# Kernel tuning notes

Measured on AMD Instinct MI355X. Metric: run time of the kernel, lower is better.

## Reference

```python
import jax, jax.numpy as jnp
import numpy as np

B, S, D, E = 4, 4096, 2048, 64
NOISE_STD = 1.0


def setup_inputs() -> dict:
    key = jax.random.key(0)
    k1, k2, k3, k4 = jax.random.split(key, 4)
    x = jax.random.normal(k1, (B, S, D), dtype=jnp.float32)
    lim = float(np.sqrt(6.0 / (D + E)))  # glorot_uniform
    W_gate = jax.random.uniform(k2, (D, E), jnp.float32, -lim, lim)
    # keras inits noise_dense kernel to zeros; use tiny random values so the
    # noise path is numerically exercised (zeros would make it trivially ln(2)).
    W_noise = 0.02 * jax.random.normal(k3, (D, E), dtype=jnp.float32)
    noise = jax.random.normal(k4, (B * S, E), dtype=jnp.float32)
    return {"x": x, "W_gate": W_gate, "W_noise": W_noise, "noise": noise, "top_k": 2}


def reference(x, W_gate, W_noise, noise, top_k):
    b, s, d = x.shape
    e = W_gate.shape[1]
    xf = x.reshape(-1, d)                         # [N, D], N = b*s
    gate_logits = xf @ W_gate                     # [N, E]
    # training-mode noise injection
    noise_logits = xf @ W_noise                   # [N, E]
    nstd = jax.nn.softplus(noise_logits) * (NOISE_STD / (e * e))
    gate_logits = gate_logits + noise * nstd
    # top-k mask + masked softmax
    top_vals, top_idx = jax.lax.top_k(gate_logits, top_k)   # [N, K]
    n = gate_logits.shape[0]
    mask = jnp.zeros_like(gate_logits).at[jnp.arange(n)[:, None], top_idx].set(1.0)
    masked_logits = jnp.where(mask > 0, gate_logits, jnp.float32(-1e9))
    expert_weights = jax.nn.softmax(masked_logits, axis=-1)  # [N, E]
    raw_gate_probs = jax.nn.softmax(gate_logits, axis=-1)    # [N, E]
    expert_weights = expert_weights.reshape(b, s, e)
    expert_indices = top_idx.reshape(b, s, top_k).astype(jnp.int32)
    return expert_weights, expert_indices, gate_logits, raw_gate_probs
```

## Files before the change

kernel.cpp:

```cpp
#include <hip/hip_runtime.h>
#include <math.h>


typedef _Float16 f16;
typedef f16  f16x8  __attribute__((ext_vector_type(8)));
typedef float f32x16 __attribute__((ext_vector_type(16)));

constexpr int NROWS = 16384;
constexpr int DDIM  = 2048;
constexpr int NE    = 64;
constexpr int BM    = 32;
constexpr int KI    = 32;
constexpr int NITER = DDIM / KI;
constexpr float NSCALE = 1.0f / 4096.0f;

__device__ __forceinline__ float softplus_f(float x) {
    return fmaxf(x, 0.0f) + log1pf(expf(-fabsf(x)));
}

__device__ __forceinline__ int a_off(int buf, int v, int s) {
    return ((buf * 2 + v) * 2 + s) * 1024;
}
__device__ __forceinline__ int b_off(int buf, int v, int f, int s) {
    return 8192 + (((buf * 2 + v) * 4 + f) * 2 + s) * 1024;
}

__device__ __forceinline__ void gload_lds16(const void* g, void* l) {
    __builtin_amdgcn_global_load_lds(
        (const __attribute__((address_space(1))) void*)g,
        (__attribute__((address_space(3))) void*)l, 16, 0, 0);
}

__global__ __launch_bounds__(256) void wprep_kernel(
    const float* __restrict__ Wg, const float* __restrict__ Wn,
    f16* __restrict__ ws)
{
    int t = blockIdx.x * 256 + threadIdx.x;
    int S = t >> 8;
    int f = (t >> 6) & 3;
    int l = t & 63;
    int k0  = S * 16 + (l >> 5) * 8;
    int col = f * 32 + (l & 31);
    const float* src = (col < NE) ? (Wg + col) : (Wn + col - NE);
    f16x8 hp, lp;
    #pragma unroll
    for (int j = 0; j < 8; ++j) {
        float w  = src[(size_t)(k0 + j) * NE];
        f16 h    = (f16)w;
        float hf = (float)h;
        hp[j] = h;
        lp[j] = (f16)((w - hf) * 64.0f);
    }
    size_t base = (size_t)(S * 4 + f) * 1024;
    *(f16x8*)(ws + base + l * 8)       = hp;
    *(f16x8*)(ws + base + 512 + l * 8) = lp;
}

__global__ __launch_bounds__(256, 2) void gemm_gating(
    const float* __restrict__ x, const f16* __restrict__ wfrag,
    const float* __restrict__ noise,
    float* __restrict__ out_w, float* __restrict__ out_idx,
    float* __restrict__ out_logits, float* __restrict__ out_probs)
{
    __shared__ char smem[40960];
    const int tid = threadIdx.x;
    const int l   = tid & 63;
    const int w   = tid >> 6;
    const int row0 = blockIdx.x * BM;

    f32x16 acc1, acc2;
    #pragma unroll
    for (int r = 0; r < 16; ++r) { acc1[r] = 0.0f; acc2[r] = 0.0f; }

    const int sA   = w;
    const int sr   = l & 31;
    const int kg   = sA * 2 + (l >> 5);
    const float* xrow = x + (size_t)(row0 + sr) * DDIM + kg * 8;

    float4 xv0, xv1;
    auto stageA_load = [&](int i) {
        if (w < 2) {
            xv0 = *(const float4*)(xrow + i * KI);
            xv1 = *(const float4*)(xrow + i * KI + 4);
        }
    };
    auto stageA_write = [&](int buf) {
        if (w < 2) {
            float xs[8] = {xv0.x, xv0.y, xv0.z, xv0.w, xv1.x, xv1.y, xv1.z, xv1.w};
            f16x8 hp, lp;
            #pragma unroll
            for (int j = 0; j < 8; ++j) {
                f16 h    = (f16)xs[j];
                float hf = (float)h;
                hp[j] = h;
                lp[j] = (f16)((xs[j] - hf) * 64.0f);
            }
            *(f16x8*)(smem + a_off(buf, 0, sA) + l * 16) = hp;
            *(f16x8*)(smem + a_off(buf, 1, sA) + l * 16) = lp;
        }
    };
    auto stageB = [&](int i, int buf) {
        #pragma unroll
        for (int v = 0; v < 2; ++v)
            #pragma unroll
            for (int s = 0; s < 2; ++s) {
                int S = i * 2 + s;
                const f16* src = wfrag + (size_t)(S * 4 + w) * 1024 + v * 512 + l * 8;
                gload_lds16(src, smem + b_off(buf, v, w, s));
            }
    };
    auto compute = [&](int buf) {
        #pragma unroll
        for (int s = 0; s < 2; ++s) {
            f16x8 Ah = *(const f16x8*)(smem + a_off(buf, 0, s) + l * 16);
            f16x8 Al = *(const f16x8*)(smem + a_off(buf, 1, s) + l * 16);
            f16x8 Bh = *(const f16x8*)(smem + b_off(buf, 0, w, s) + l * 16);
            f16x8 Bl = *(const f16x8*)(smem + b_off(buf, 1, w, s) + l * 16);
            acc1 = __builtin_amdgcn_mfma_f32_32x32x16_f16(Ah, Bh, acc1, 0, 0, 0);
            acc2 = __builtin_amdgcn_mfma_f32_32x32x16_f16(Ah, Bl, acc2, 0, 0, 0);
            acc2 = __builtin_amdgcn_mfma_f32_32x32x16_f16(Al, Bh, acc2, 0, 0, 0);
        }
    };

    stageA_load(0);
    stageB(0, 0);
    stageA_write(0);
    __syncthreads();

    for (int i = 0; i < NITER; ++i) {
        int buf = i & 1;
        bool more = (i + 1 < NITER);
        if (more) { stageA_load(i + 1); stageB(i + 1, buf ^ 1); }
        compute(buf);
        if (more) stageA_write(buf ^ 1);
        __syncthreads();
    }

    float* lgf = (float*)smem;
    #pragma unroll
    for (int r = 0; r < 16; ++r) {
        float cv = fmaf(acc2[r], 0.015625f, acc1[r]);
        int row = (r & 3) + 8 * (r >> 2) + 4 * (l >> 5);
        int col = w * 32 + (l & 31);
        lgf[row * 132 + col] = cv;
    }
    __syncthreads();

    {
        const int pr = tid & 31;
        const int c8 = tid >> 5;
        const int n1 = row0 + pr;
        const float4* gl4 = (const float4*)(lgf + pr * 132 + c8 * 8);
        const float4* nl4 = (const float4*)(lgf + pr * 132 + 64 + c8 * 8);
        const float4* nz4 = (const float4*)(noise + (size_t)n1 * NE + c8 * 8);
        float4* gw4 = (float4*)(lgf + pr * 132 + c8 * 8);
        float4* ol4 = (float4*)(out_logits + (size_t)n1 * NE + c8 * 8);
        #pragma unroll
        for (int q = 0; q < 2; ++q) {
            float4 G = gl4[q], NL = nl4[q], NZ = nz4[q];
            G.x += NZ.x * softplus_f(NL.x) * NSCALE;
            G.y += NZ.y * softplus_f(NL.y) * NSCALE;
            G.z += NZ.z * softplus_f(NL.z) * NSCALE;
            G.w += NZ.w * softplus_f(NL.w) * NSCALE;
            gw4[q] = G;
            ol4[q] = G;
        }
    }
    __syncthreads();

    {
        const int g2   = l >> 3;
        const int c    = l & 7;
        const int row2 = w * 8 + g2;
        const int n2   = row0 + row2;

        float mv[8];
        {
            const float4* mr = (const float4*)(lgf + row2 * 132 + c * 8);
            float4 m0 = mr[0], m1 = mr[1];
            mv[0]=m0.x; mv[1]=m0.y; mv[2]=m0.z; mv[3]=m0.w;
            mv[4]=m1.x; mv[5]=m1.y; mv[6]=m1.z; mv[7]=m1.w;
        }
        float v0 = -INFINITY, v1 = -INFINITY;
        int i0 = 0, i1 = 0;
        #pragma unroll
        for (int j = 0; j < 8; ++j) {
            float v = mv[j]; int e = c * 8 + j;
            if (v > v0) { v1 = v0; i1 = i0; v0 = v; i0 = e; }
            else if (v > v1) { v1 = v; i1 = e; }
        }
        #pragma unroll
        for (int m = 1; m <= 4; m <<= 1) {
            float ov0 = __shfl_xor(v0, m), ov1 = __shfl_xor(v1, m);
            int   oi0 = __shfl_xor(i0, m), oi1 = __shfl_xor(i1, m);
            if (ov0 > v0) {
                bool keep = (v0 > ov1);
                v1 = keep ? v0 : ov1; i1 = keep ? i0 : oi1;
                v0 = ov0; i0 = oi0;
            } else if (ov0 > v1) {
                v1 = ov0; i1 = oi0;
            }
        }
        const int srcl = l & 56;
        v0 = __shfl(v0, srcl); i0 = __shfl(i0, srcl);
        v1 = __shfl(v1, srcl); i1 = __shfl(i1, srcl);

        float se = 0.0f;
        #pragma unroll
        for (int j = 0; j < 8; ++j) se += expf(mv[j] - v0);
        se += __shfl_xor(se, 1); se += __shfl_xor(se, 2); se += __shfl_xor(se, 4);
        float inv_se = 1.0f / se;

        float t  = expf(v1 - v0);
        float w0 = 1.0f / (1.0f + t);
        float w1 = t * w0;

        float pr[8], wt[8];
        #pragma unroll
        for (int j = 0; j < 8; ++j) {
            int e = c * 8 + j;
            pr[j] = expf(mv[j] - v0) * inv_se;
            wt[j] = (e == i0) ? w0 : ((e == i1) ? w1 : 0.0f);
        }
        *(float4*)(out_probs + (size_t)n2 * NE + c * 8)     = make_float4(pr[0], pr[1], pr[2], pr[3]);
        *(float4*)(out_probs + (size_t)n2 * NE + c * 8 + 4) = make_float4(pr[4], pr[5], pr[6], pr[7]);
        *(float4*)(out_w + (size_t)n2 * NE + c * 8)         = make_float4(wt[0], wt[1], wt[2], wt[3]);
        *(float4*)(out_w + (size_t)n2 * NE + c * 8 + 4)     = make_float4(wt[4], wt[5], wt[6], wt[7]);
        if (c == 0) {
            *(float2*)(out_idx + (size_t)n2 * 2) = make_float2((float)i0, (float)i1);
        }
    }
}

extern "C" void kernel_launch(void* const* d_in, const int* in_sizes, int n_in,
                              void* d_out, int out_size, void* d_ws, size_t ws_size,
                              hipStream_t stream) {
    (void)in_sizes; (void)n_in; (void)ws_size; (void)out_size;
    const float* x     = (const float*)d_in[0];
    const float* Wg    = (const float*)d_in[1];
    const float* Wn    = (const float*)d_in[2];
    const float* noise = (const float*)d_in[3];
    float* out        = (float*)d_out;
    float* out_w      = out;
    float* out_idx    = out + (size_t)NROWS * NE;
    float* out_logits = out_idx + (size_t)NROWS * 2;
    float* out_probs  = out_logits + (size_t)NROWS * NE;
    f16* wfrag = (f16*)d_ws;

    wprep_kernel<<<128, 256, 0, stream>>>(Wg, Wn, wfrag);
    gemm_gating<<<NROWS / BM, 256, 0, stream>>>(
        x, wfrag, noise, out_w, out_idx, out_logits, out_probs);
}
```

Baseline: 63.20 us.

## Replace LDS-staged double buffering with direct register loads for GEMM operands

The GEMM main loop no longer stages x and weight fragments through shared memory with per-iteration barriers. Each wave now loads its A and B fragments straight from global memory into registers, using a two-deep software prefetch, and does the fp16 hi/lo split in registers. This removes the LDS traffic and the __syncthreads in the loop. The cost is that all four waves now load the same x rows redundantly, and global-load latency is hidden only by register prefetch.

```diff
diff --git a/kernel.cpp b/kernel.cpp
--- a/kernel.cpp
+++ b/kernel.cpp
@@ -10,25 +10,11 @@
 constexpr int DDIM  = 2048;
 constexpr int NE    = 64;
 constexpr int BM    = 32;
-constexpr int KI    = 32;
-constexpr int NITER = DDIM / KI;
+constexpr int NSL   = DDIM / 16;
 constexpr float NSCALE = 1.0f / 4096.0f;
 
 __device__ __forceinline__ float softplus_f(float x) {
     return fmaxf(x, 0.0f) + log1pf(expf(-fabsf(x)));
-}
-
-__device__ __forceinline__ int a_off(int buf, int v, int s) {
-    return ((buf * 2 + v) * 2 + s) * 1024;
-}
-__device__ __forceinline__ int b_off(int buf, int v, int f, int s) {
-    return 8192 + (((buf * 2 + v) * 4 + f) * 2 + s) * 1024;
-}
-
-__device__ __forceinline__ void gload_lds16(const void* g, void* l) {
-    __builtin_amdgcn_global_load_lds(
-        (const __attribute__((address_space(1))) void*)g,
-        (__attribute__((address_space(3))) void*)l, 16, 0, 0);
 }
 
 __global__ __launch_bounds__(256) void wprep_kernel(
@@ -62,7 +48,7 @@
     float* __restrict__ out_w, float* __restrict__ out_idx,
     float* __restrict__ out_logits, float* __restrict__ out_probs)
 {
-    __shared__ char smem[40960];
+    __shared__ float lgf[BM * 132];
     const int tid = threadIdx.x;
     const int l   = tid & 63;
     const int w   = tid >> 6;
@@ -72,71 +58,52 @@
     #pragma unroll
     for (int r = 0; r < 16; ++r) { acc1[r] = 0.0f; acc2[r] = 0.0f; }
 
-    const int sA   = w;
-    const int sr   = l & 31;
-    const int kg   = sA * 2 + (l >> 5);
-    const float* xrow = x + (size_t)(row0 + sr) * DDIM + kg * 8;
-
-    float4 xv0, xv1;
-    auto stageA_load = [&](int i) {
-        if (w < 2) {
-            xv0 = *(const float4*)(xrow + i * KI);
-            xv1 = *(const float4*)(xrow + i * KI + 4);
-        }
+    const float* aptr = x + (size_t)(row0 + (l & 31)) * DDIM + ((l >> 5) * 8);
+    const f16*   bptr = wfrag + (size_t)w * 1024 + l * 8;
+
+    auto loadA = [&](int S, float4& a0, float4& a1) {
+        const float* p = aptr + S * 16;
+        a0 = *(const float4*)p;
+        a1 = *(const float4*)(p + 4);
     };
-    auto stageA_write = [&](int buf) {
-        if (w < 2) {
-            float xs[8] = {xv0.x, xv0.y, xv0.z, xv0.w, xv1.x, xv1.y, xv1.z, xv1.w};
-            f16x8 hp, lp;
-            #pragma unroll
-            for (int j = 0; j < 8; ++j) {
-                f16 h    = (f16)xs[j];
-                float hf = (float)h;
-                hp[j] = h;
-                lp[j] = (f16)((xs[j] - hf) * 64.0f);
-            }
-            *(f16x8*)(smem + a_off(buf, 0, sA) + l * 16) = hp;
-            *(f16x8*)(smem + a_off(buf, 1, sA) + l * 16) = lp;
-        }
+    auto loadB = [&](int S, f16x8& bh, f16x8& bl) {
+        const f16* p = bptr + (size_t)S * 4096;
+        bh = *(const f16x8*)p;
+        bl = *(const f16x8*)(p + 512);
     };
-    auto stageB = [&](int i, int buf) {
-        #pragma unroll
-        for (int v = 0; v < 2; ++v)
-            #pragma unroll
-            for (int s = 0; s < 2; ++s) {
-                int S = i * 2 + s;
-                const f16* src = wfrag + (size_t)(S * 4 + w) * 1024 + v * 512 + l * 8;
-                gload_lds16(src, smem + b_off(buf, v, w, s));
-            }
+    auto compute = [&](const float4& a0, const float4& a1,
+                       const f16x8& bh, const f16x8& bl) {
+        float xs[8] = {a0.x, a0.y, a0.z, a0.w, a1.x, a1.y, a1.z, a1.w};
+        f16x8 Ah, Al;
+        #pragma unroll
+        for (int j = 0; j < 8; ++j) {
+            f16 h    = (f16)xs[j];
+            float hf = (float)h;
+            Ah[j] = h;
+            Al[j] = (f16)((xs[j] - hf) * 64.0f);
+        }
+        acc1 = __builtin_amdgcn_mfma_f32_32x32x16_f16(Ah, bh, acc1, 0, 0, 0);
+        acc2 = __builtin_amdgcn_mfma_f32_32x32x16_f16(Ah, bl, acc2, 0, 0, 0);
+        acc2 = __builtin_amdgcn_mfma_f32_32x32x16_f16(Al, bh, acc2, 0, 0, 0);
     };
-    auto compute = [&](int buf) {
-        #pragma unroll
-        for (int s = 0; s < 2; ++s) {
-            f16x8 Ah = *(const f16x8*)(smem + a_off(buf, 0, s) + l * 16);
-            f16x8 Al = *(const f16x8*)(smem + a_off(buf, 1, s) + l * 16);
-            f16x8 Bh = *(const f16x8*)(smem + b_off(buf, 0, w, s) + l * 16);
-            f16x8 Bl = *(const f16x8*)(smem + b_off(buf, 1, w, s) + l * 16);
-            acc1 = __builtin_amdgcn_mfma_f32_32x32x16_f16(Ah, Bh, acc1, 0, 0, 0);
-            acc2 = __builtin_amdgcn_mfma_f32_32x32x16_f16(Ah, Bl, acc2, 0, 0, 0);
-            acc2 = __builtin_amdgcn_mfma_f32_32x32x16_f16(Al, Bh, acc2, 0, 0, 0);
-        }
-    };
-
-    stageA_load(0);
-    stageB(0, 0);
-    stageA_write(0);
-    __syncthreads();
-
-    for (int i = 0; i < NITER; ++i) {
-        int buf = i & 1;
-        bool more = (i + 1 < NITER);
-        if (more) { stageA_load(i + 1); stageB(i + 1, buf ^ 1); }
-        compute(buf);
-        if (more) stageA_write(buf ^ 1);
-        __syncthreads();
-    }
-
-    float* lgf = (float*)smem;
+
+    float4 ra0, ra1, sa0, sa1;
+    f16x8  rbh, rbl, sbh, sbl;
+    loadA(0, ra0, ra1);
+    loadB(0, rbh, rbl);
+
+    #pragma unroll 2
+    for (int t = 0; t < NSL / 2; ++t) {
+        loadA(2 * t + 1, sa0, sa1);
+        loadB(2 * t + 1, sbh, sbl);
+        compute(ra0, ra1, rbh, rbl);
+        if (t + 1 < NSL / 2) {
+            loadA(2 * t + 2, ra0, ra1);
+            loadB(2 * t + 2, rbh, rbl);
+        }
+        compute(sa0, sa1, sbh, sbl);
+    }
+
     #pragma unroll
     for (int r = 0; r < 16; ++r) {
         float cv = fmaf(acc2[r], 0.015625f, acc1[r]);
```

Result: slower. 88.84 us (+40.6%).

## Triple-buffer LDS pipeline with explicit vmcnt waits and split barriers

Applied to the files above, without the earlier changes.

Switches the main GEMM loop from double to triple buffering in LDS, prefetching the A and B tiles two iterations ahead. Hand-placed s_waitcnt vmcnt counts and sched barriers let async global-to-LDS loads stay in flight across barriers instead of draining every iteration. This raises LDS use from 40 KB to 60 KB per block, which may limit the two-blocks-per-CU occupancy target. It also relies on exact in-flight load counts being correct for each wave type.

```diff
diff --git a/kernel.cpp b/kernel.cpp
--- a/kernel.cpp
+++ b/kernel.cpp
@@ -19,16 +19,38 @@
 }
 
 __device__ __forceinline__ int a_off(int buf, int v, int s) {
-    return ((buf * 2 + v) * 2 + s) * 1024;
+    return buf * 4096 + (v * 2 + s) * 1024;
 }
 __device__ __forceinline__ int b_off(int buf, int v, int f, int s) {
-    return 8192 + (((buf * 2 + v) * 4 + f) * 2 + s) * 1024;
+    return 12288 + buf * 16384 + (((v * 4) + f) * 2 + s) * 1024;
 }
 
 __device__ __forceinline__ void gload_lds16(const void* g, void* l) {
     __builtin_amdgcn_global_load_lds(
         (const __attribute__((address_space(1))) void*)g,
         (__attribute__((address_space(3))) void*)l, 16, 0, 0);
+}
+
+__device__ __forceinline__ void barrier_close() {
+    asm volatile("s_waitcnt lgkmcnt(0)" ::: "memory");
+    __builtin_amdgcn_sched_barrier(0);
+    __builtin_amdgcn_s_barrier();
+    asm volatile("" ::: "memory");
+}
+__device__ __forceinline__ void barrier_publish_steady(bool heavy) {
+    if (heavy) asm volatile("s_waitcnt vmcnt(6) lgkmcnt(0)" ::: "memory");
+    else       asm volatile("s_waitcnt vmcnt(4) lgkmcnt(0)" ::: "memory");
+    __builtin_amdgcn_sched_barrier(0);
+    __builtin_amdgcn_s_barrier();
+    asm volatile("" ::: "memory");
+    __builtin_amdgcn_sched_barrier(0);
+}
+__device__ __forceinline__ void barrier_publish_drain() {
+    asm volatile("s_waitcnt vmcnt(0) lgkmcnt(0)" ::: "memory");
+    __builtin_amdgcn_sched_barrier(0);
+    __builtin_amdgcn_s_barrier();
+    asm volatile("" ::: "memory");
+    __builtin_amdgcn_sched_barrier(0);
 }
 
 __global__ __launch_bounds__(256) void wprep_kernel(
@@ -62,31 +84,29 @@
     float* __restrict__ out_w, float* __restrict__ out_idx,
     float* __restrict__ out_logits, float* __restrict__ out_probs)
 {
-    __shared__ char smem[40960];
+    __shared__ __align__(16) char smem[61440];
     const int tid = threadIdx.x;
     const int l   = tid & 63;
     const int w   = tid >> 6;
+    const bool heavy = (w < 2);
     const int row0 = blockIdx.x * BM;
 
     f32x16 acc1, acc2;
     #pragma unroll
     for (int r = 0; r < 16; ++r) { acc1[r] = 0.0f; acc2[r] = 0.0f; }
 
-    const int sA   = w;
-    const int sr   = l & 31;
-    const int kg   = sA * 2 + (l >> 5);
-    const float* xrow = x + (size_t)(row0 + sr) * DDIM + kg * 8;
-
-    float4 xv0, xv1;
-    auto stageA_load = [&](int i) {
-        if (w < 2) {
-            xv0 = *(const float4*)(xrow + i * KI);
-            xv1 = *(const float4*)(xrow + i * KI + 4);
-        }
-    };
-    auto stageA_write = [&](int buf) {
-        if (w < 2) {
-            float xs[8] = {xv0.x, xv0.y, xv0.z, xv0.w, xv1.x, xv1.y, xv1.z, xv1.w};
+    const float* xrow = x + (size_t)(row0 + (l & 31)) * DDIM + w * 16 + (l >> 5) * 8;
+
+    auto loadA = [&](int i, float4& a0, float4& a1) {
+        if (heavy) {
+            const float* p = xrow + i * KI;
+            a0 = *(const float4*)p;
+            a1 = *(const float4*)(p + 4);
+        }
+    };
+    auto writeA = [&](const float4& a0, const float4& a1, int buf) {
+        if (heavy) {
+            float xs[8] = {a0.x, a0.y, a0.z, a0.w, a1.x, a1.y, a1.z, a1.w};
             f16x8 hp, lp;
             #pragma unroll
             for (int j = 0; j < 8; ++j) {
@@ -95,8 +115,8 @@
                 hp[j] = h;
                 lp[j] = (f16)((xs[j] - hf) * 64.0f);
             }
-            *(f16x8*)(smem + a_off(buf, 0, sA) + l * 16) = hp;
-            *(f16x8*)(smem + a_off(buf, 1, sA) + l * 16) = lp;
+            *(f16x8*)(smem + a_off(buf, 0, w) + l * 16) = hp;
+            *(f16x8*)(smem + a_off(buf, 1, w) + l * 16) = lp;
         }
     };
     auto stageB = [&](int i, int buf) {
@@ -122,19 +142,29 @@
         }
     };
 
-    stageA_load(0);
+    float4 t0a, t0b, nxt0, nxt1;
+    loadA(0, t0a, t0b);
     stageB(0, 0);
-    stageA_write(0);
+    loadA(1, nxt0, nxt1);
+    stageB(1, 1);
+    writeA(t0a, t0b, 0);
+
+    int b0 = 0, b1 = 1, b2 = 2;
+    for (int t = 0; t < NITER; ++t) {
+        barrier_close();
+        float4 ld0 = nxt0, ld1 = nxt1;
+        if (t + 2 < NITER) {
+            stageB(t + 2, b2);
+            loadA(t + 2, ld0, ld1);
+        }
+        if (t + 1 < NITER) writeA(nxt0, nxt1, b1);
+        nxt0 = ld0; nxt1 = ld1;
+        if (t + 2 < NITER) barrier_publish_steady(heavy);
+        else               barrier_publish_drain();
+        compute(b0);
+        int tmp = b0; b0 = b1; b1 = b2; b2 = tmp;
+    }
     __syncthreads();
-
-    for (int i = 0; i < NITER; ++i) {
-        int buf = i & 1;
-        bool more = (i + 1 < NITER);
-        if (more) { stageA_load(i + 1); stageB(i + 1, buf ^ 1); }
-        compute(buf);
-        if (more) stageA_write(buf ^ 1);
-        __syncthreads();
-    }
 
     float* lgf = (float*)smem;
     #pragma unroll
```

Result: faster. 57.94 us (-8.3%).

## Stream fp32 x tiles directly to LDS with a 4-stage async pipeline

Applied to the files above, without the earlier changes.

Replaces the register-staged x load and early fp16 split with direct global-to-LDS loads of raw fp32 x. The hi/lo split now happens in the compute step after reading LDS. The kernel uses a four-buffer ring with three tiles in flight, gated by explicit vmcnt waits and raw barriers, to hide global latency. LDS doubles to 80KB, which may limit occupancy to one block per CU despite the launch bound of 2. The split conversion is now redone by all four waves instead of two.

```diff
diff --git a/kernel.cpp b/kernel.cpp
--- a/kernel.cpp
+++ b/kernel.cpp
@@ -14,15 +14,16 @@
 constexpr int NITER = DDIM / KI;
 constexpr float NSCALE = 1.0f / 4096.0f;
 
+constexpr int BUFSZ = 20480;
+__device__ __forceinline__ int a_off(int buf, int s, int j4) {
+    return buf * BUFSZ + (s * 2 + j4) * 1024;
+}
+__device__ __forceinline__ int b_off(int buf, int v, int f, int s) {
+    return buf * BUFSZ + 4096 + ((v * 4 + f) * 2 + s) * 1024;
+}
+
 __device__ __forceinline__ float softplus_f(float x) {
     return fmaxf(x, 0.0f) + log1pf(expf(-fabsf(x)));
-}
-
-__device__ __forceinline__ int a_off(int buf, int v, int s) {
-    return ((buf * 2 + v) * 2 + s) * 1024;
-}
-__device__ __forceinline__ int b_off(int buf, int v, int f, int s) {
-    return 8192 + (((buf * 2 + v) * 4 + f) * 2 + s) * 1024;
 }
 
 __device__ __forceinline__ void gload_lds16(const void* g, void* l) {
@@ -30,6 +31,13 @@
         (const __attribute__((address_space(1))) void*)g,
         (__attribute__((address_space(3))) void*)l, 16, 0, 0);
 }
+
+#define PIPE_BAR(N) do {                                                   \
+    asm volatile("s_waitcnt vmcnt(" #N ") lgkmcnt(0)" ::: "memory");       \
+    __builtin_amdgcn_sched_barrier(0);                                     \
+    __builtin_amdgcn_s_barrier();                                          \
+    __builtin_amdgcn_sched_barrier(0);                                     \
+} while (0)
 
 __global__ __launch_bounds__(256) void wprep_kernel(
     const float* __restrict__ Wg, const float* __restrict__ Wn,
@@ -62,7 +70,7 @@
     float* __restrict__ out_w, float* __restrict__ out_idx,
     float* __restrict__ out_logits, float* __restrict__ out_probs)
 {
-    __shared__ char smem[40960];
+    __shared__ __align__(16) char smem[81920];
     const int tid = threadIdx.x;
     const int l   = tid & 63;
     const int w   = tid >> 6;
@@ -72,48 +80,33 @@
     #pragma unroll
     for (int r = 0; r < 16; ++r) { acc1[r] = 0.0f; acc2[r] = 0.0f; }
 
-    const int sA   = w;
-    const int sr   = l & 31;
-    const int kg   = sA * 2 + (l >> 5);
-    const float* xrow = x + (size_t)(row0 + sr) * DDIM + kg * 8;
-
-    float4 xv0, xv1;
-    auto stageA_load = [&](int i) {
-        if (w < 2) {
-            xv0 = *(const float4*)(xrow + i * KI);
-            xv1 = *(const float4*)(xrow + i * KI + 4);
-        }
+    const float* aSrc = x + (size_t)(row0 + (l & 31)) * DDIM
+                          + (w >> 1) * 16 + (l >> 5) * 8 + (w & 1) * 4;
+    const f16* bSrc = wfrag + (size_t)w * 1024 + l * 8;
+
+    auto stage = [&](int t, int buf) {
+        gload_lds16(aSrc + (size_t)t * KI, smem + a_off(buf, w >> 1, w & 1));
+        #pragma unroll
+        for (int v = 0; v < 2; ++v)
+            #pragma unroll
+            for (int s = 0; s < 2; ++s)
+                gload_lds16(bSrc + (size_t)(t * 2 + s) * 4096 + v * 512,
+                            smem + b_off(buf, v, w, s));
     };
-    auto stageA_write = [&](int buf) {
-        if (w < 2) {
-            float xs[8] = {xv0.x, xv0.y, xv0.z, xv0.w, xv1.x, xv1.y, xv1.z, xv1.w};
-            f16x8 hp, lp;
+    auto compute = [&](int buf) {
+        #pragma unroll
+        for (int s = 0; s < 2; ++s) {
+            float4 a0 = *(const float4*)(smem + a_off(buf, s, 0) + l * 16);
+            float4 a1 = *(const float4*)(smem + a_off(buf, s, 1) + l * 16);
+            float xs[8] = {a0.x, a0.y, a0.z, a0.w, a1.x, a1.y, a1.z, a1.w};
+            f16x8 Ah, Al;
             #pragma unroll
             for (int j = 0; j < 8; ++j) {
                 f16 h    = (f16)xs[j];
                 float hf = (float)h;
-                hp[j] = h;
-                lp[j] = (f16)((xs[j] - hf) * 64.0f);
+                Ah[j] = h;
+                Al[j] = (f16)((xs[j] - hf) * 64.0f);
             }
-            *(f16x8*)(smem + a_off(buf, 0, sA) + l * 16) = hp;
-            *(f16x8*)(smem + a_off(buf, 1, sA) + l * 16) = lp;
-        }
-    };
-    auto stageB = [&](int i, int buf) {
-        #pragma unroll
-        for (int v = 0; v < 2; ++v)
-            #pragma unroll
-            for (int s = 0; s < 2; ++s) {
-                int S = i * 2 + s;
-                const f16* src = wfrag + (size_t)(S * 4 + w) * 1024 + v * 512 + l * 8;
-                gload_lds16(src, smem + b_off(buf, v, w, s));
-            }
-    };
-    auto compute = [&](int buf) {
-        #pragma unroll
-        for (int s = 0; s < 2; ++s) {
-            f16x8 Ah = *(const f16x8*)(smem + a_off(buf, 0, s) + l * 16);
-            f16x8 Al = *(const f16x8*)(smem + a_off(buf, 1, s) + l * 16);
             f16x8 Bh = *(const f16x8*)(smem + b_off(buf, 0, w, s) + l * 16);
             f16x8 Bl = *(const f16x8*)(smem + b_off(buf, 1, w, s) + l * 16);
             acc1 = __builtin_amdgcn_mfma_f32_32x32x16_f16(Ah, Bh, acc1, 0, 0, 0);
@@ -122,19 +115,20 @@
         }
     };
 
-    stageA_load(0);
-    stageB(0, 0);
-    stageA_write(0);
+    stage(0, 0);
+    stage(1, 1);
+    stage(2, 2);
+
+    for (int t = 0; t < NITER - 2; ++t) {
+        PIPE_BAR(10);
+        if (t + 3 < NITER) stage(t + 3, (t + 3) & 3);
+        compute(t & 3);
+    }
+    PIPE_BAR(5);
+    compute((NITER - 2) & 3);
+    PIPE_BAR(0);
+    compute((NITER - 1) & 3);
     __syncthreads();
-
-    for (int i = 0; i < NITER; ++i) {
-        int buf = i & 1;
-        bool more = (i + 1 < NITER);
-        if (more) { stageA_load(i + 1); stageB(i + 1, buf ^ 1); }
-        compute(buf);
-        if (more) stageA_write(buf ^ 1);
-        __syncthreads();
-    }
 
     float* lgf = (float*)smem;
     #pragma unroll
```

After: 69.19 us. +9.5%, slower.
